# Optimization experiments

Measured on AMD Instinct MI355X. Metric: run time of the kernel, lower is better.

## Reference

```python
import jax, jax.numpy as jnp
import numpy as np

V, D, L, H, F, K, T_MAX = 50265, 768, 12, 12, 3072, 2, 512
DH = D // H
EPS = 1e-12


def _ln(x, w, b):
    mu = jnp.mean(x, axis=-1, keepdims=True)
    var = jnp.mean(jnp.square(x - mu), axis=-1, keepdims=True)
    return (x - mu) * jax.lax.rsqrt(var + EPS) * w + b


def setup_inputs() -> dict:
    key = jax.random.key(0)
    ks = iter(jax.random.split(key, 32))
    B, T = 8, 512
    inp = {}
    inp['input_ids'] = jax.random.randint(next(ks), (B, T), 0, V, dtype=jnp.int64)
    inp['attention_mask'] = jnp.ones((B, T), dtype=jnp.int32)
    s = 0.02
    inp['tok_emb'] = jax.random.normal(next(ks), (V, D), jnp.float32) * s
    inp['pos_emb'] = jax.random.normal(next(ks), (T_MAX, D), jnp.float32) * s
    inp['lang_emb'] = jax.random.normal(next(ks), (K, D), jnp.float32) * s
    inp['switch_emb'] = jax.random.normal(next(ks), (D,), jnp.float32) * s
    # prototypes: orthogonal-ish rows scaled by 0.5
    P = jax.random.normal(next(ks), (K, D), jnp.float32)
    Pq, _ = jnp.linalg.qr(P.T)  # (D, K) orthonormal cols
    inp['prototypes'] = Pq.T * 0.5
    inp['log_tau'] = jnp.array(0.0, jnp.float32)  # log(1.0)
    inp['emb_ln_w'] = jnp.ones((D,), jnp.float32)
    inp['emb_ln_b'] = jnp.zeros((D,), jnp.float32)
    # per-layer params, stacked with leading L dim; Linear weights stored torch-style (out,in)
    inp['Wq'] = jax.random.normal(next(ks), (L, D, D), jnp.float32) * s
    inp['Wk'] = jax.random.normal(next(ks), (L, D, D), jnp.float32) * s
    inp['Wv'] = jax.random.normal(next(ks), (L, D, D), jnp.float32) * s
    inp['Wo'] = jax.random.normal(next(ks), (L, D, D), jnp.float32) * s
    inp['Wo_b'] = jnp.zeros((L, D), jnp.float32)
    inp['compat'] = jnp.broadcast_to(jnp.eye(K), (L, H, K, K)) + 0.01 * jax.random.normal(next(ks), (L, H, K, K), jnp.float32)
    inp['gamma'] = jnp.zeros((L,), jnp.float32)
    inp['W1'] = jax.random.normal(next(ks), (L, F, D), jnp.float32) * s
    inp['b1'] = jnp.zeros((L, F), jnp.float32)
    inp['W2'] = jax.random.normal(next(ks), (L, D, F), jnp.float32) * s
    inp['b2'] = jnp.zeros((L, D), jnp.float32)
    inp['ln1_w'] = jnp.ones((L, D), jnp.float32)
    inp['ln1_b'] = jnp.zeros((L, D), jnp.float32)
    inp['ln2_w'] = jnp.ones((L, D), jnp.float32)
    inp['ln2_b'] = jnp.zeros((L, D), jnp.float32)
    return inp


def reference(input_ids, attention_mask, tok_emb, pos_emb, lang_emb, switch_emb,
              prototypes, log_tau, emb_ln_w, emb_ln_b,
              Wq, Wk, Wv, Wo, Wo_b, compat, gamma,
              W1, b1, W2, b2, ln1_w, ln1_b, ln2_w, ln2_b):
    B, T = input_ids.shape
    # Stage 1: raw base embedding (tok + pos)
    h_base = tok_emb[input_ids] + pos_emb[jnp.arange(T)][None, :, :]  # (B,T,D)
    # pre-contextual language distributions p0 and switch magnitudes s
    tau = jnp.maximum(jnp.exp(log_tau), 0.25)
    p = jax.nn.softmax(jnp.einsum('btd,kd->btk', h_base, prototypes) / tau, axis=-1)  # (B,T,K)
    sim = jnp.sum(p[:, 1:] * p[:, :-1], axis=-1)
    s = jnp.concatenate([jnp.zeros((B, 1), p.dtype), 1.0 - sim], axis=1)  # (B,T)
    # Stage 2: augment + LN (dropout is identity in eval)
    h = _ln(h_base + p @ lang_emb + s[..., None] * switch_emb, emb_ln_w, emb_ln_b)
    additive = (1.0 - attention_mask.astype(h.dtype))[:, None, None, :] * -10000.0  # (B,1,1,T)
    scale = 1.0 / np.sqrt(DH)
    for l in range(L):
        q = jnp.einsum('btd,ed->bte', h, Wq[l]).reshape(B, T, H, DH).transpose(0, 2, 1, 3)
        k = jnp.einsum('btd,ed->bte', h, Wk[l]).reshape(B, T, H, DH).transpose(0, 2, 1, 3)
        v = jnp.einsum('btd,ed->bte', h, Wv[l]).reshape(B, T, H, DH).transpose(0, 2, 1, 3)
        scores = jnp.einsum('bhid,bhjd->bhij', q, k) * scale
        # per-head language compatibility bias p_i^T C_h p_j
        p_compat = jnp.einsum('bik,hkl->bhil', p, compat[l])
        scores = scores + jnp.einsum('bhil,bjl->bhij', p_compat, p)
        scores = scores + gamma[l] * s[:, None, None, :]
        scores = scores + additive
        attn = jax.nn.softmax(scores, axis=-1)
        ctx = jnp.einsum('bhij,bhjd->bhid', attn, v).transpose(0, 2, 1, 3).reshape(B, T, D)
        attn_out = jnp.einsum('btd,ed->bte', ctx, Wo[l]) + Wo_b[l]
        h_mid = _ln(h + attn_out, ln1_w[l], ln1_b[l])
        ffn = jnp.einsum('btf,df->btd', jax.nn.gelu(jnp.einsum('btd,fd->btf', h_mid, W1[l]) + b1[l], approximate=False), W2[l]) + b2[l]
        h = _ln(h_mid + ffn, ln2_w[l], ln2_b[l])
    return h
```

## Files before the change

### kernel.cpp

```cpp
#include <hip/hip_runtime.h>
#include <hip/hip_bf16.h>
#include <math.h>


typedef __bf16 bf16;
typedef __attribute__((ext_vector_type(8))) __bf16 bf16x8;
typedef __attribute__((ext_vector_type(4))) __bf16 bf16x4;
typedef __attribute__((ext_vector_type(4))) float f32x4;

#define N_TOK 4096
#define D_SZ 768
#define F_SZ 3072
#define L_SZ 12
#define MN_SZ ((size_t)N_TOK * D_SZ)

__device__ __forceinline__ void async_ld16(const void* g, void* l) {
  __builtin_amdgcn_global_load_lds((const __attribute__((address_space(1))) void*)g,
                                   (__attribute__((address_space(3))) void*)l, 16, 0, 0);
}

__device__ inline void block_reduce2(float& a, float& b, int tid) {
  #pragma unroll
  for (int off = 32; off; off >>= 1) {
    a += __shfl_xor(a, off);
    b += __shfl_xor(b, off);
  }
  __shared__ float red[8];
  if ((tid & 63) == 0) { red[tid >> 6] = a; red[4 + (tid >> 6)] = b; }
  __syncthreads();
  a = red[0] + red[1] + red[2] + red[3];
  b = red[4] + red[5] + red[6] + red[7];
  __syncthreads();
}

__global__ void __launch_bounds__(256) f2b_kernel(const float* __restrict__ src,
                                                  bf16* __restrict__ dst, int n4) {
  int i = blockIdx.x * 256 + threadIdx.x;
  if (i >= n4) return;
  float4 v = ((const float4*)src)[i];
  bf16x4 o; o.x = (bf16)v.x; o.y = (bf16)v.y; o.z = (bf16)v.z; o.w = (bf16)v.w;
  *(bf16x4*)(dst + (size_t)i * 4) = o;
}

__global__ void __launch_bounds__(256) build_wqkv_kernel(const float* __restrict__ Wq,
    const float* __restrict__ Wk, const float* __restrict__ Wv, bf16* __restrict__ dst) {
  int i = blockIdx.x * 256 + threadIdx.x;
  const int per_layer = 2304 * 768;
  long idx = (long)i * 4;
  if (idx >= 12L * per_layer) return;
  int l = (int)(idx / per_layer);
  int rem = (int)(idx - (long)l * per_layer);
  int r = rem / 768;
  int c = rem - r * 768;
  const float* src;
  if (r < 768)       src = Wq + ((size_t)l * 768 + r) * 768 + c;
  else if (r < 1536) src = Wk + ((size_t)l * 768 + (r - 768)) * 768 + c;
  else               src = Wv + ((size_t)l * 768 + (r - 1536)) * 768 + c;
  float4 v = *(const float4*)src;
  bf16x4 o; o.x = (bf16)v.x; o.y = (bf16)v.y; o.z = (bf16)v.z; o.w = (bf16)v.w;
  *(bf16x4*)(dst + idx) = o;
}

__global__ void __launch_bounds__(256) embed_a_kernel(const int* __restrict__ ids,
    const float* __restrict__ tok, const float* __restrict__ pos,
    const float* __restrict__ proto, const float* __restrict__ log_tau,
    float* __restrict__ h_base, float* __restrict__ p_out) {
  int n = blockIdx.x;
  int t = n & 511;
  int tid = threadIdx.x;
  int id = ids[n];
  float d0 = 0.f, d1 = 0.f;
  #pragma unroll
  for (int jj = 0; jj < 3; jj++) {
    int j = tid + jj * 256;
    float v = tok[(size_t)id * 768 + j] + pos[(size_t)t * 768 + j];
    h_base[(size_t)n * 768 + j] = v;
    d0 += v * proto[j];
    d1 += v * proto[768 + j];
  }
  block_reduce2(d0, d1, tid);
  if (tid == 0) {
    float tau = fmaxf(__expf(log_tau[0]), 0.25f);
    float a = d0 / tau, bb = d1 / tau;
    float m = fmaxf(a, bb);
    float e0 = __expf(a - m), e1 = __expf(bb - m);
    float si = e0 + e1;
    p_out[n * 2] = e0 / si;
    p_out[n * 2 + 1] = e1 / si;
  }
}

__global__ void __launch_bounds__(256) embed_c_kernel(const float* __restrict__ h_base,
    const float* __restrict__ p, const float* __restrict__ lang, const float* __restrict__ sw,
    const float* __restrict__ lw, const float* __restrict__ lb,
    float* __restrict__ s_out, float* __restrict__ h_out, bf16* __restrict__ h_bf) {
  int n = blockIdx.x;
  int t = n & 511;
  int tid = threadIdx.x;
  float p0 = p[n * 2], p1 = p[n * 2 + 1];
  float sv = 0.f;
  if (t > 0) sv = 1.f - (p0 * p[(n - 1) * 2] + p1 * p[(n - 1) * 2 + 1]);
  if (tid == 0) s_out[n] = sv;
  float x[3]; float sum = 0.f, sq = 0.f;
  #pragma unroll
  for (int jj = 0; jj < 3; jj++) {
    int j = tid + jj * 256;
    float v = h_base[(size_t)n * 768 + j] + p0 * lang[j] + p1 * lang[768 + j] + sv * sw[j];
    x[jj] = v; sum += v; sq += v * v;
  }
  block_reduce2(sum, sq, tid);
  float mean = sum * (1.f / 768.f);
  float var = fmaxf(sq * (1.f / 768.f) - mean * mean, 0.f);
  float inv = rsqrtf(var + 1e-12f);
  #pragma unroll
  for (int jj = 0; jj < 3; jj++) {
    int j = tid + jj * 256;
    float o = (x[jj] - mean) * inv * lw[j] + lb[j];
    h_out[(size_t)n * 768 + j] = o;
    h_bf[(size_t)n * 768 + j] = (bf16)o;
  }
}

__global__ void __launch_bounds__(256) ln3_kernel(const float* __restrict__ x1,
    const float* __restrict__ x2, const float* __restrict__ x3, const float* __restrict__ bias,
    const float* __restrict__ w, const float* __restrict__ bv,
    float* __restrict__ out_f, bf16* __restrict__ out_b) {
  int n = blockIdx.x;
  int tid = threadIdx.x;
  float x[3]; float sum = 0.f, sq = 0.f;
  #pragma unroll
  for (int jj = 0; jj < 3; jj++) {
    int j = tid + jj * 256;
    size_t o = (size_t)n * 768 + j;
    float v = x1[o] + x2[o] + x3[o] + bias[j];
    x[jj] = v; sum += v; sq += v * v;
  }
  block_reduce2(sum, sq, tid);
  float mean = sum * (1.f / 768.f);
  float var = fmaxf(sq * (1.f / 768.f) - mean * mean, 0.f);
  float inv = rsqrtf(var + 1e-12f);
  #pragma unroll
  for (int jj = 0; jj < 3; jj++) {
    int j = tid + jj * 256;
    float o = (x[jj] - mean) * inv * w[j] + bv[j];
    out_f[(size_t)n * 768 + j] = o;
    out_b[(size_t)n * 768 + j] = (bf16)o;
  }
}

template <int MODE>
__global__ void __launch_bounds__(256) gemm_nt(const bf16* __restrict__ A,
    const bf16* __restrict__ B, void* __restrict__ C, bf16* __restrict__ C2,
    const float* __restrict__ bias, int M, int N, int K) {
  __shared__ bf16 As[128 * 32];
  __shared__ bf16 Bs[128 * 32];
  const int tid = threadIdx.x;
  const int lane = tid & 63;
  const int wave = tid >> 6;
  const int wm = wave >> 1, wn = wave & 1;
  const int m0 = blockIdx.x * 128, n0 = blockIdx.y * 128;
  const int fr = lane & 15, fq = lane >> 4;
  const int srow = wave * 16 + (lane >> 2);
  const int scol = (lane & 3) * 8;

  int kb = 0, ke = K;
  if (MODE == 1) { int half = K >> 1; kb = blockIdx.z * half; ke = kb + half; }

  f32x4 acc[4][4] = {};
  const bf16* Ap = A + (size_t)(m0 + srow) * K + scol;
  const bf16* Bp = B + (size_t)(n0 + srow) * K + scol;
  bf16* AsW = &As[wave * 512];
  bf16* BsW = &Bs[wave * 512];
  for (int k0 = kb; k0 < ke; k0 += 32) {
    async_ld16(Ap + k0, AsW);
    async_ld16(Ap + (size_t)64 * K + k0, AsW + 64 * 32);
    async_ld16(Bp + k0, BsW);
    async_ld16(Bp + (size_t)64 * K + k0, BsW + 64 * 32);
    __syncthreads();
    bf16x8 af[4], bfr[4];
    #pragma unroll
    for (int i = 0; i < 4; i++) af[i]  = *(const bf16x8*)&As[(wm * 64 + i * 16 + fr) * 32 + fq * 8];
    #pragma unroll
    for (int i = 0; i < 4; i++) bfr[i] = *(const bf16x8*)&Bs[(wn * 64 + i * 16 + fr) * 32 + fq * 8];
    #pragma unroll
    for (int i = 0; i < 4; i++)
      #pragma unroll
      for (int j = 0; j < 4; j++)
        acc[i][j] = __builtin_amdgcn_mfma_f32_16x16x32_bf16(af[i], bfr[j], acc[i][j], 0, 0, 0);
    __syncthreads();
  }

  const bool vregion = (MODE == 3) && (n0 >= 1536);
  float* Cz = (MODE == 1) ? ((float*)C + (size_t)blockIdx.z * M * N) : (float*)C;
  #pragma unroll
  for (int i = 0; i < 4; i++) {
    int row0 = m0 + wm * 64 + i * 16 + fq * 4;
    #pragma unroll
    for (int j = 0; j < 4; j++) {
      int col = n0 + wn * 64 + j * 16 + fr;
      if (MODE == 3 && vregion) {
        int vcol = col - 1536;
        int h = vcol >> 6, dh = vcol & 63;
        int b = row0 >> 9, t0 = row0 & 511;
        bf16x4 o;
        #pragma unroll
        for (int r = 0; r < 4; r++) o[r] = (bf16)acc[i][j][r];
        *(bf16x4*)&C2[((size_t)(b * 12 + h) * 64 + dh) * 512 + t0] = o;
      } else {
        #pragma unroll
        for (int r = 0; r < 4; r++) {
          float v = acc[i][j][r];
          if (MODE == 2) {
            v += bias[col];
            v = 0.5f * v * (1.f + erff(v * 0.70710678118654752f));
          }
          if (MODE == 1)      Cz[(size_t)(row0 + r) * N + col] = v;
          else if (MODE == 3) ((bf16*)C)[(size_t)(row0 + r) * 1536 + col] = (bf16)v;
          else                ((bf16*)C)[(size_t)(row0 + r) * N + col] = (bf16)v;
        }
      }
    }
  }
}

__global__ void __launch_bounds__(256) attn_kernel(const bf16* __restrict__ qkv,
    const bf16* __restrict__ vt, const float* __restrict__ p, const float* __restrict__ s,
    const int* __restrict__ mask, const float* __restrict__ compat,
    const float* __restrict__ gamma, int l, bf16* __restrict__ ctx) {
  __shared__ float scb[32 * 512];
  const int tid = threadIdx.x;
  const int lane = tid & 63;
  const int w = tid >> 6;
  const int fr = lane & 15, fq = lane >> 4;
  const int qc = blockIdx.x, h = blockIdx.y, b = blockIdx.z;
  const int i0 = qc * 32;
  const float* Cm = compat + (size_t)(l * 12 + h) * 4;
  const float gl = gamma[l];

  bf16x8 qf[2][2];
  #pragma unroll
  for (int mt = 0; mt < 2; mt++)
    #pragma unroll
    for (int kk = 0; kk < 2; kk++)
      qf[mt][kk] = *(const bf16x8*)&qkv[(size_t)(b * 512 + i0 + mt * 16 + fr) * 1536 + h * 64 + kk * 32 + fq * 8];
  for (int ntl = 0; ntl < 8; ++ntl) {
    int j0 = (w * 8 + ntl) * 16;
    bf16x8 kf0 = *(const bf16x8*)&qkv[(size_t)(b * 512 + j0 + fr) * 1536 + 768 + h * 64 + fq * 8];
    bf16x8 kf1 = *(const bf16x8*)&qkv[(size_t)(b * 512 + j0 + fr) * 1536 + 768 + h * 64 + 32 + fq * 8];
    #pragma unroll
    for (int mt = 0; mt < 2; mt++) {
      f32x4 acc = {};
      acc = __builtin_amdgcn_mfma_f32_16x16x32_bf16(qf[mt][0], kf0, acc, 0, 0, 0);
      acc = __builtin_amdgcn_mfma_f32_16x16x32_bf16(qf[mt][1], kf1, acc, 0, 0, 0);
      #pragma unroll
      for (int r = 0; r < 4; r++)
        scb[(mt * 16 + fq * 4 + r) * 512 + j0 + fr] = acc[r] * 0.125f;
    }
  }
  __syncthreads();

  for (int il = 0; il < 8; ++il) {
    int i = w * 8 + il;
    int qi = i0 + i;
    float p0 = p[(b * 512 + qi) * 2], p1 = p[(b * 512 + qi) * 2 + 1];
    float cp0 = p0 * Cm[0] + p1 * Cm[2];
    float cp1 = p0 * Cm[1] + p1 * Cm[3];
    float x[8]; float mx = -3.0e38f;
    #pragma unroll
    for (int jj = 0; jj < 8; jj++) {
      int j = lane + jj * 64;
      float pj0 = p[(b * 512 + j) * 2], pj1 = p[(b * 512 + j) * 2 + 1];
      float add = (1.f - (float)mask[b * 512 + j]) * -10000.f;
      float v = scb[i * 512 + j] + cp0 * pj0 + cp1 * pj1 + gl * s[b * 512 + j] + add;
      x[jj] = v; mx = fmaxf(mx, v);
    }
    #pragma unroll
    for (int off = 32; off; off >>= 1) mx = fmaxf(mx, __shfl_xor(mx, off));
    float sum = 0.f;
    #pragma unroll
    for (int jj = 0; jj < 8; jj++) { float e = __expf(x[jj] - mx); x[jj] = e; sum += e; }
    #pragma unroll
    for (int off = 32; off; off >>= 1) sum += __shfl_xor(sum, off);
    float inv = 1.f / sum;
    #pragma unroll
    for (int jj = 0; jj < 8; jj++) scb[i * 512 + lane + jj * 64] = x[jj] * inv;
  }
  __syncthreads();

  const int mt = w & 1;
  const int ntb = (w >> 1) * 2;
  f32x4 acc[2] = {};
  for (int kt = 0; kt < 16; ++kt) {
    bf16x8 af;
    const float* prow = &scb[(mt * 16 + fr) * 512 + kt * 32 + fq * 8];
    #pragma unroll
    for (int jj = 0; jj < 8; jj++) af[jj] = (bf16)prow[jj];
    #pragma unroll
    for (int np = 0; np < 2; np++) {
      bf16x8 vf = *(const bf16x8*)&vt[(size_t)((b * 12 + h) * 64 + (ntb + np) * 16 + fr) * 512 + kt * 32 + fq * 8];
      acc[np] = __builtin_amdgcn_mfma_f32_16x16x32_bf16(af, vf, acc[np], 0, 0, 0);
    }
  }
  #pragma unroll
  for (int np = 0; np < 2; np++)
    #pragma unroll
    for (int r = 0; r < 4; r++)
      ctx[(size_t)(b * 512 + i0 + mt * 16 + fq * 4 + r) * 768 + h * 64 + (ntb + np) * 16 + fr] = (bf16)acc[np][r];
}

extern "C" void kernel_launch(void* const* d_in, const int* in_sizes, int n_in,
                              void* d_out, int out_size, void* d_ws, size_t ws_size,
                              hipStream_t stream) {
  const int*   input_ids  = (const int*)d_in[0];
  const int*   attn_mask  = (const int*)d_in[1];
  const float* tok_emb    = (const float*)d_in[2];
  const float* pos_emb    = (const float*)d_in[3];
  const float* lang_emb   = (const float*)d_in[4];
  const float* switch_emb = (const float*)d_in[5];
  const float* prototypes = (const float*)d_in[6];
  const float* log_tau    = (const float*)d_in[7];
  const float* emb_ln_w   = (const float*)d_in[8];
  const float* emb_ln_b   = (const float*)d_in[9];
  const float* Wq   = (const float*)d_in[10];
  const float* Wk   = (const float*)d_in[11];
  const float* Wv   = (const float*)d_in[12];
  const float* Wo   = (const float*)d_in[13];
  const float* Wo_b = (const float*)d_in[14];
  const float* compat = (const float*)d_in[15];
  const float* gamma  = (const float*)d_in[16];
  const float* W1   = (const float*)d_in[17];
  const float* b1   = (const float*)d_in[18];
  const float* W2   = (const float*)d_in[19];
  const float* b2   = (const float*)d_in[20];
  const float* ln1_w = (const float*)d_in[21];
  const float* ln1_b = (const float*)d_in[22];
  const float* ln2_w = (const float*)d_in[23];
  const float* ln2_b = (const float*)d_in[24];

  char* wsp = (char*)d_ws;
  size_t off = 0;
  auto alloc = [&](size_t bytes) { void* pp = wsp + off; off += (bytes + 255) & ~(size_t)255; return pp; };
  float* h_f      = (float*)alloc(MN_SZ * 4);
  bf16*  h_bf     = (bf16*)alloc(MN_SZ * 2);
  float* h_base   = (float*)alloc(MN_SZ * 4);
  float* h_mid    = (float*)alloc(MN_SZ * 4);
  bf16*  h_mid_bf = (bf16*)alloc(MN_SZ * 2);
  float* tmp      = (float*)alloc(MN_SZ * 4 * 2);
  float* p_buf    = (float*)alloc((size_t)N_TOK * 2 * 4);
  float* s_buf    = (float*)alloc((size_t)N_TOK * 4);
  bf16*  qkv      = (bf16*)alloc((size_t)N_TOK * 1536 * 2);
  bf16*  vt       = (bf16*)alloc(MN_SZ * 2);
  bf16*  ctx      = (bf16*)alloc(MN_SZ * 2);
  bf16*  a1       = (bf16*)alloc((size_t)N_TOK * F_SZ * 2);
  bf16*  wqkv_bf  = (bf16*)alloc((size_t)L_SZ * 2304 * 768 * 2);
  bf16*  wo_bf    = (bf16*)alloc((size_t)L_SZ * 768 * 768 * 2);
  bf16*  w1_bf    = (bf16*)alloc((size_t)L_SZ * 3072 * 768 * 2);
  bf16*  w2_bf    = (bf16*)alloc((size_t)L_SZ * 768 * 3072 * 2);
  (void)ws_size; (void)in_sizes; (void)n_in; (void)out_size;

  build_wqkv_kernel<<<(12 * 2304 * 768 / 4 + 255) / 256, 256, 0, stream>>>(Wq, Wk, Wv, wqkv_bf);
  f2b_kernel<<<(12 * 768 * 768 / 4 + 255) / 256, 256, 0, stream>>>(Wo, wo_bf, 12 * 768 * 768 / 4);
  f2b_kernel<<<(12 * 3072 * 768 / 4 + 255) / 256, 256, 0, stream>>>(W1, w1_bf, 12 * 3072 * 768 / 4);
  f2b_kernel<<<(12 * 768 * 3072 / 4 + 255) / 256, 256, 0, stream>>>(W2, w2_bf, 12 * 768 * 3072 / 4);

  embed_a_kernel<<<N_TOK, 256, 0, stream>>>(input_ids, tok_emb, pos_emb, prototypes, log_tau,
                                            h_base, p_buf);
  embed_c_kernel<<<N_TOK, 256, 0, stream>>>(h_base, p_buf, lang_emb, switch_emb, emb_ln_w,
                                            emb_ln_b, s_buf, h_f, h_bf);

  for (int l = 0; l < 12; ++l) {
    gemm_nt<3><<<dim3(32, 18), 256, 0, stream>>>(h_bf, wqkv_bf + (size_t)l * 2304 * 768, qkv,
                                                 vt, nullptr, N_TOK, 2304, 768);
    attn_kernel<<<dim3(16, 12, 8), 256, 0, stream>>>(qkv, vt, p_buf, s_buf, attn_mask,
                                                     compat, gamma, l, ctx);
    gemm_nt<1><<<dim3(32, 6, 2), 256, 0, stream>>>(ctx, wo_bf + (size_t)l * 768 * 768, tmp,
                                                   nullptr, nullptr, N_TOK, 768, 768);
    ln3_kernel<<<N_TOK, 256, 0, stream>>>(h_f, tmp, tmp + MN_SZ, Wo_b + l * 768,
                                          ln1_w + l * 768, ln1_b + l * 768, h_mid, h_mid_bf);
    gemm_nt<2><<<dim3(32, 24), 256, 0, stream>>>(h_mid_bf, w1_bf + (size_t)l * 3072 * 768, a1,
                                                 nullptr, b1 + l * 3072, N_TOK, 3072, 768);
    gemm_nt<1><<<dim3(32, 6, 2), 256, 0, stream>>>(a1, w2_bf + (size_t)l * 768 * 3072, tmp,
                                                   nullptr, nullptr, N_TOK, 768, 3072);
    float* hdst = (l == 11) ? (float*)d_out : h_f;
    ln3_kernel<<<N_TOK, 256, 0, stream>>>(h_mid, tmp, tmp + MN_SZ, b2 + l * 768,
                                          ln2_w + l * 768, ln2_b + l * 768, hdst, h_bf);
  }
}
```

Before: 3.103 ms.

## Split-K four ways for output GEMMs and rework attention softmax LDS layout

The Wo and W2 GEMMs now split K across four z-slices instead of two, writing four fp32 partials that a new LayerNorm kernel sums, which raises block count to fill more compute units. The cost is extra partial-buffer writes and reads. The attention kernel pads its score rows to avoid LDS bank conflicts and hoists the per-key bias terms out of the row loop. It also keeps softmax results in registers and writes them back once as bf16, so the PV MFMA loads packed vectors instead of converting floats. h_base is aliased into the enlarged tmp buffer to save workspace.

New measurement: 2.868 ms. -7.6%, faster.

```diff
diff --git a/kernel.cpp b/kernel.cpp
--- a/kernel.cpp
+++ b/kernel.cpp
@@ -13,6 +13,8 @@
 #define F_SZ 3072
 #define L_SZ 12
 #define MN_SZ ((size_t)N_TOK * D_SZ)
+#define SPITCH 516
+#define PPITCH 520
 
 __device__ __forceinline__ void async_ld16(const void* g, void* l) {
   __builtin_amdgcn_global_load_lds((const __attribute__((address_space(1))) void*)g,
@@ -121,8 +123,8 @@
   }
 }
 
-__global__ void __launch_bounds__(256) ln3_kernel(const float* __restrict__ x1,
-    const float* __restrict__ x2, const float* __restrict__ x3, const float* __restrict__ bias,
+__global__ void __launch_bounds__(256) ln5_kernel(const float* __restrict__ x1,
+    const float* __restrict__ t, const float* __restrict__ bias,
     const float* __restrict__ w, const float* __restrict__ bv,
     float* __restrict__ out_f, bf16* __restrict__ out_b) {
   int n = blockIdx.x;
@@ -132,7 +134,7 @@
   for (int jj = 0; jj < 3; jj++) {
     int j = tid + jj * 256;
     size_t o = (size_t)n * 768 + j;
-    float v = x1[o] + x2[o] + x3[o] + bias[j];
+    float v = x1[o] + (t[o] + t[o + MN_SZ]) + (t[o + 2 * MN_SZ] + t[o + 3 * MN_SZ]) + bias[j];
     x[jj] = v; sum += v; sq += v * v;
   }
   block_reduce2(sum, sq, tid);
@@ -164,7 +166,7 @@
   const int scol = (lane & 3) * 8;
 
   int kb = 0, ke = K;
-  if (MODE == 1) { int half = K >> 1; kb = blockIdx.z * half; ke = kb + half; }
+  if (MODE == 1) { int ks = K / gridDim.z; kb = blockIdx.z * ks; ke = kb + ks; }
 
   f32x4 acc[4][4] = {};
   const bf16* Ap = A + (size_t)(m0 + srow) * K + scol;
@@ -227,7 +229,7 @@
     const bf16* __restrict__ vt, const float* __restrict__ p, const float* __restrict__ s,
     const int* __restrict__ mask, const float* __restrict__ compat,
     const float* __restrict__ gamma, int l, bf16* __restrict__ ctx) {
-  __shared__ float scb[32 * 512];
+  __shared__ float scb[32 * SPITCH];
   const int tid = threadIdx.x;
   const int lane = tid & 63;
   const int w = tid >> 6;
@@ -254,58 +256,71 @@
       acc = __builtin_amdgcn_mfma_f32_16x16x32_bf16(qf[mt][1], kf1, acc, 0, 0, 0);
       #pragma unroll
       for (int r = 0; r < 4; r++)
-        scb[(mt * 16 + fq * 4 + r) * 512 + j0 + fr] = acc[r] * 0.125f;
+        scb[(mt * 16 + fq * 4 + r) * SPITCH + j0 + fr] = acc[r] * 0.125f;
     }
   }
+
+  float pj0[8], pj1[8], basej[8];
+  #pragma unroll
+  for (int jj = 0; jj < 8; jj++) {
+    int j = lane + jj * 64;
+    pj0[jj] = p[(b * 512 + j) * 2];
+    pj1[jj] = p[(b * 512 + j) * 2 + 1];
+    basej[jj] = gl * s[b * 512 + j] + (1.f - (float)mask[b * 512 + j]) * -10000.f;
+  }
   __syncthreads();
 
+  float xs[8][8];
+  #pragma unroll
   for (int il = 0; il < 8; ++il) {
     int i = w * 8 + il;
     int qi = i0 + i;
     float p0 = p[(b * 512 + qi) * 2], p1 = p[(b * 512 + qi) * 2 + 1];
     float cp0 = p0 * Cm[0] + p1 * Cm[2];
     float cp1 = p0 * Cm[1] + p1 * Cm[3];
-    float x[8]; float mx = -3.0e38f;
+    float mx = -3.0e38f;
     #pragma unroll
     for (int jj = 0; jj < 8; jj++) {
-      int j = lane + jj * 64;
-      float pj0 = p[(b * 512 + j) * 2], pj1 = p[(b * 512 + j) * 2 + 1];
-      float add = (1.f - (float)mask[b * 512 + j]) * -10000.f;
-      float v = scb[i * 512 + j] + cp0 * pj0 + cp1 * pj1 + gl * s[b * 512 + j] + add;
-      x[jj] = v; mx = fmaxf(mx, v);
+      float v = scb[i * SPITCH + lane + jj * 64] + cp0 * pj0[jj] + cp1 * pj1[jj] + basej[jj];
+      xs[il][jj] = v; mx = fmaxf(mx, v);
     }
     #pragma unroll
     for (int off = 32; off; off >>= 1) mx = fmaxf(mx, __shfl_xor(mx, off));
     float sum = 0.f;
     #pragma unroll
-    for (int jj = 0; jj < 8; jj++) { float e = __expf(x[jj] - mx); x[jj] = e; sum += e; }
+    for (int jj = 0; jj < 8; jj++) { float e = __expf(xs[il][jj] - mx); xs[il][jj] = e; sum += e; }
     #pragma unroll
     for (int off = 32; off; off >>= 1) sum += __shfl_xor(sum, off);
     float inv = 1.f / sum;
     #pragma unroll
-    for (int jj = 0; jj < 8; jj++) scb[i * 512 + lane + jj * 64] = x[jj] * inv;
+    for (int jj = 0; jj < 8; jj++) xs[il][jj] *= inv;
   }
   __syncthreads();
 
-  const int mt = w & 1;
+  bf16* pbf = (bf16*)scb;
+  #pragma unroll
+  for (int il = 0; il < 8; ++il)
+    #pragma unroll
+    for (int jj = 0; jj < 8; jj++)
+      pbf[(w * 8 + il) * PPITCH + lane + jj * 64] = (bf16)xs[il][jj];
+  __syncthreads();
+
+  const int mt3 = w & 1;
   const int ntb = (w >> 1) * 2;
-  f32x4 acc[2] = {};
+  f32x4 acc3[2] = {};
   for (int kt = 0; kt < 16; ++kt) {
-    bf16x8 af;
-    const float* prow = &scb[(mt * 16 + fr) * 512 + kt * 32 + fq * 8];
-    #pragma unroll
-    for (int jj = 0; jj < 8; jj++) af[jj] = (bf16)prow[jj];
+    bf16x8 af = *(const bf16x8*)&pbf[(mt3 * 16 + fr) * PPITCH + kt * 32 + fq * 8];
     #pragma unroll
     for (int np = 0; np < 2; np++) {
       bf16x8 vf = *(const bf16x8*)&vt[(size_t)((b * 12 + h) * 64 + (ntb + np) * 16 + fr) * 512 + kt * 32 + fq * 8];
-      acc[np] = __builtin_amdgcn_mfma_f32_16x16x32_bf16(af, vf, acc[np], 0, 0, 0);
+      acc3[np] = __builtin_amdgcn_mfma_f32_16x16x32_bf16(af, vf, acc3[np], 0, 0, 0);
     }
   }
   #pragma unroll
   for (int np = 0; np < 2; np++)
     #pragma unroll
     for (int r = 0; r < 4; r++)
-      ctx[(size_t)(b * 512 + i0 + mt * 16 + fq * 4 + r) * 768 + h * 64 + (ntb + np) * 16 + fr] = (bf16)acc[np][r];
+      ctx[(size_t)(b * 512 + i0 + mt3 * 16 + fq * 4 + r) * 768 + h * 64 + (ntb + np) * 16 + fr] = (bf16)acc3[np][r];
 }
 
 extern "C" void kernel_launch(void* const* d_in, const int* in_sizes, int n_in,
@@ -342,10 +357,10 @@
   auto alloc = [&](size_t bytes) { void* pp = wsp + off; off += (bytes + 255) & ~(size_t)255; return pp; };
   float* h_f      = (float*)alloc(MN_SZ * 4);
   bf16*  h_bf     = (bf16*)alloc(MN_SZ * 2);
-  float* h_base   = (float*)alloc(MN_SZ * 4);
   float* h_mid    = (float*)alloc(MN_SZ * 4);
   bf16*  h_mid_bf = (bf16*)alloc(MN_SZ * 2);
-  float* tmp      = (float*)alloc(MN_SZ * 4 * 2);
+  float* tmp      = (float*)alloc(MN_SZ * 4 * 4);
+  float* h_base   = tmp + 3 * MN_SZ;
   float* p_buf    = (float*)alloc((size_t)N_TOK * 2 * 4);
   float* s_buf    = (float*)alloc((size_t)N_TOK * 4);
   bf16*  qkv      = (bf16*)alloc((size_t)N_TOK * 1536 * 2);
@@ -373,16 +388,16 @@
                                                  vt, nullptr, N_TOK, 2304, 768);
     attn_kernel<<<dim3(16, 12, 8), 256, 0, stream>>>(qkv, vt, p_buf, s_buf, attn_mask,
                                                      compat, gamma, l, ctx);
-    gemm_nt<1><<<dim3(32, 6, 2), 256, 0, stream>>>(ctx, wo_bf + (size_t)l * 768 * 768, tmp,
+    gemm_nt<1><<<dim3(32, 6, 4), 256, 0, stream>>>(ctx, wo_bf + (size_t)l * 768 * 768, tmp,
                                                    nullptr, nullptr, N_TOK, 768, 768);
-    ln3_kernel<<<N_TOK, 256, 0, stream>>>(h_f, tmp, tmp + MN_SZ, Wo_b + l * 768,
+    ln5_kernel<<<N_TOK, 256, 0, stream>>>(h_f, tmp, Wo_b + l * 768,
                                           ln1_w + l * 768, ln1_b + l * 768, h_mid, h_mid_bf);
     gemm_nt<2><<<dim3(32, 24), 256, 0, stream>>>(h_mid_bf, w1_bf + (size_t)l * 3072 * 768, a1,
                                                  nullptr, b1 + l * 3072, N_TOK, 3072, 768);
-    gemm_nt<1><<<dim3(32, 6, 2), 256, 0, stream>>>(a1, w2_bf + (size_t)l * 768 * 3072, tmp,
+    gemm_nt<1><<<dim3(32, 6, 4), 256, 0, stream>>>(a1, w2_bf + (size_t)l * 768 * 3072, tmp,
                                                    nullptr, nullptr, N_TOK, 768, 3072);
     float* hdst = (l == 11) ? (float*)d_out : h_f;
-    ln3_kernel<<<N_TOK, 256, 0, stream>>>(h_mid, tmp, tmp + MN_SZ, b2 + l * 768,
+    ln5_kernel<<<N_TOK, 256, 0, stream>>>(h_mid, tmp, b2 + l * 768,
                                           ln2_w + l * 768, ln2_b + l * 768, hdst, h_bf);
   }
 }
```
